# Performance work log

Measured on AMD Instinct MI355X. Metric: run time of the kernel, lower is better.

Reference implementation:

```python
import jax, jax.numpy as jnp
import numpy as np

B, C, L = 16, 128, 2048


def setup_inputs() -> dict:
    key = jax.random.key(0)
    ks = jax.random.split(key, 7)
    s = 1.0 / np.sqrt(C)  # torch Conv1d default init scale
    x = jax.random.normal(ks[0], (B, C, L), dtype=jnp.float32)
    W1 = jax.random.uniform(ks[1], (C, C), jnp.float32, -s, s)
    b1 = jax.random.uniform(ks[2], (C,), jnp.float32, -s, s)
    W2 = jax.random.uniform(ks[3], (C, C), jnp.float32, -s, s)
    b2 = jax.random.uniform(ks[4], (C,), jnp.float32, -s, s)
    W3 = jax.random.uniform(ks[5], (C, C), jnp.float32, -s, s)
    b3 = jax.random.uniform(ks[6], (C,), jnp.float32, -s, s)
    return {"x": x, "W1": W1, "b1": b1, "W2": W2, "b2": b2, "W3": W3, "b3": b3}


def _conv1x1(x, W, b):
    # x: [B,C,L], W: [out,in] -> [B,out,L]
    return jnp.einsum('oc,bcl->bol', W, x) + b[None, :, None]


def reference(x, W1, b1, W2, b2, W3, b3):
    q = _conv1x1(x, W1, b1).transpose(0, 2, 1)  # [B,L,C]
    k = _conv1x1(x, W2, b2).transpose(0, 2, 1)  # [B,L,C]
    v = _conv1x1(x, W3, b3).transpose(0, 2, 1)  # [B,L,C]
    attn = jnp.einsum('bic,bjc->bij', q, k)     # [B,L,L]
    attn = jax.nn.softmax(attn, axis=-1)
    out = jnp.einsum('bij,bjc->bic', attn, v)   # [B,L,C]
    return out.transpose(0, 2, 1)               # [B,C,L]
```

## Files before the change

### kernel.cpp

```cpp
#include <hip/hip_runtime.h>
#include <hip/hip_bf16.h>
#include <stdint.h>

#define B_ 16
#define C_ 128
#define L_ 2048
#define LOG2E 1.4426950408889634f

typedef __attribute__((ext_vector_type(8))) short bf16x8;
typedef __attribute__((ext_vector_type(4))) float f32x4;
typedef __attribute__((ext_vector_type(16))) float f32x16;
typedef __attribute__((ext_vector_type(4))) unsigned int u32x4;

typedef __attribute__((address_space(3))) unsigned int lds_u32_t;
typedef const __attribute__((address_space(1))) unsigned int gbl_u32_t;

__device__ __forceinline__ void gload_lds16(const void* g, void* l) {
  __builtin_amdgcn_global_load_lds((gbl_u32_t*)g,
                                   (lds_u32_t*)(unsigned long long)l, 16, 0, 0);
}

__device__ __forceinline__ unsigned short f2bf(float x) {
  union { float f; unsigned u; } v; v.f = x;
  unsigned u = v.u;
  u += 0x7fffu + ((u >> 16) & 1u);
  return (unsigned short)(u >> 16);
}

__device__ __forceinline__ unsigned pk2(float a, float b) {
  return (unsigned)f2bf(a) | ((unsigned)f2bf(b) << 16);
}

__device__ __forceinline__ unsigned cvtpk_bf16(float lo, float hi_) {
  unsigned r;
  asm("v_cvt_pk_bf16_f32 %0, %1, %2" : "=v"(r) : "v"(lo), "v"(hi_));
  return r;
}

__device__ __forceinline__ f32x16 z16() {
  f32x16 v;
#pragma unroll
  for (int i = 0; i < 16; ++i) v[i] = 0.f;
  return v;
}

__device__ __forceinline__ float tmax16(f32x16 v) {
  float a0 = fmaxf(v[0], v[1]),  a1 = fmaxf(v[2], v[3]);
  float a2 = fmaxf(v[4], v[5]),  a3 = fmaxf(v[6], v[7]);
  float a4 = fmaxf(v[8], v[9]),  a5 = fmaxf(v[10], v[11]);
  float a6 = fmaxf(v[12], v[13]), a7 = fmaxf(v[14], v[15]);
  float b0 = fmaxf(a0, a1), b1 = fmaxf(a2, a3);
  float b2 = fmaxf(a4, a5), b3 = fmaxf(a6, a7);
  return fmaxf(fmaxf(b0, b1), fmaxf(b2, b3));
}

__device__ __forceinline__ float tsum16(f32x16 v) {
  float a0 = v[0] + v[1],  a1 = v[2] + v[3];
  float a2 = v[4] + v[5],  a3 = v[6] + v[7];
  float a4 = v[8] + v[9],  a5 = v[10] + v[11];
  float a6 = v[12] + v[13], a7 = v[14] + v[15];
  float b0 = a0 + a1, b1 = a2 + a3, b2 = a4 + a5, b3 = a6 + a7;
  return (b0 + b1) + (b2 + b3);
}

__global__ __launch_bounds__(256, 2) void proj_kernel(
    const float* __restrict__ x,
    const float* __restrict__ W1, const float* __restrict__ b1,
    const float* __restrict__ W2, const float* __restrict__ b2,
    const float* __restrict__ W3, const float* __restrict__ b3,
    unsigned short* __restrict__ Qo, unsigned short* __restrict__ Ko,
    unsigned short* __restrict__ Vt)
{
  __shared__ unsigned short Xt[64][136];
  __shared__ unsigned short Wl[128][136];

  const int b  = blockIdx.x & 15;
  const int lt = blockIdx.x >> 4;
  const int l0 = lt * 64;
  const int tid = threadIdx.x;
  const int w = tid >> 6, lane = tid & 63, li = lane & 15, lg = lane >> 4;

  for (int it = 0; it < 8; ++it) {
    int idx = tid + it * 256;
    int c = idx >> 4, f4 = idx & 15;
    const float4 vv = *(const float4*)(x + (size_t)(b * C_ + c) * L_ + l0 + f4 * 4);
    Xt[f4 * 4 + 0][c] = f2bf(vv.x);
    Xt[f4 * 4 + 1][c] = f2bf(vv.y);
    Xt[f4 * 4 + 2][c] = f2bf(vv.z);
    Xt[f4 * 4 + 3][c] = f2bf(vv.w);
  }

  auto stageW = [&](const float* W) {
    for (int it = 0; it < 16; ++it) {
      int idx = tid + it * 256;
      int o = idx >> 5, f4 = idx & 31;
      const float4 vv = *(const float4*)(W + (size_t)o * C_ + f4 * 4);
      unsigned short* p = &Wl[o][f4 * 4];
      p[0] = f2bf(vv.x); p[1] = f2bf(vv.y); p[2] = f2bf(vv.z); p[3] = f2bf(vv.w);
    }
  };

  auto computePhase = [&](const float* bias, unsigned short* Out, int mode, float sc) {
    f32x4 acc[8];
#pragma unroll
    for (int ni = 0; ni < 8; ++ni) acc[ni] = (f32x4){0.f, 0.f, 0.f, 0.f};
    bf16x8 af[4];
#pragma unroll
    for (int kk = 0; kk < 4; ++kk)
      af[kk] = *(const bf16x8*)&Xt[w * 16 + li][lg * 8 + kk * 32];
#pragma unroll
    for (int kk = 0; kk < 4; ++kk) {
#pragma unroll
      for (int ni = 0; ni < 8; ++ni) {
        bf16x8 bf = *(const bf16x8*)&Wl[ni * 16 + li][lg * 8 + kk * 32];
        acc[ni] = __builtin_amdgcn_mfma_f32_16x16x32_bf16(af[kk], bf, acc[ni], 0, 0, 0);
      }
    }
    if (mode == 0) {
#pragma unroll
      for (int ni = 0; ni < 8; ++ni) {
        float bv = bias[ni * 16 + li];
#pragma unroll
        for (int r = 0; r < 4; ++r) {
          int lrow = l0 + w * 16 + lg * 4 + r;
          Out[(size_t)(b * L_ + lrow) * C_ + ni * 16 + li] = f2bf((acc[ni][r] + bv) * sc);
        }
      }
    } else {
#pragma unroll
      for (int ni = 0; ni < 8; ++ni) {
        float bv = bias[ni * 16 + li];
        int o = ni * 16 + li;
        unsigned long long pw =
            (unsigned long long)pk2(acc[ni][0] + bv, acc[ni][1] + bv) |
            ((unsigned long long)pk2(acc[ni][2] + bv, acc[ni][3] + bv) << 32);
        *(unsigned long long*)(Out + (size_t)(b * C_ + o) * L_ + l0 + w * 16 + lg * 4) = pw;
      }
    }
  };

  stageW(W1);
  __syncthreads();
  computePhase(b1, Qo, 0, LOG2E);
  __syncthreads();
  stageW(W2);
  __syncthreads();
  computePhase(b2, Ko, 0, 1.0f);
  __syncthreads();
  stageW(W3);
  __syncthreads();
  computePhase(b3, Vt, 1, 1.0f);
}

__global__ __launch_bounds__(256, 1) void attn_kernel(
    const unsigned short* __restrict__ Q,
    const unsigned short* __restrict__ K,
    const unsigned short* __restrict__ Vt,
    float* __restrict__ out)
{
  __shared__ unsigned short kbuf[2][64 * C_];
  __shared__ unsigned short vbuf[2][C_ * 64];

  const int b  = blockIdx.x & 15;
  const int qt = blockIdx.x >> 4;
  const int tid = threadIdx.x;
  const int w = tid >> 6, lane = tid & 63;
  const int q32 = lane & 31, hi = lane >> 5;
  const int qrow = qt * 128 + w * 32 + q32;
  const size_t bLC = (size_t)b * L_ * C_;

  bf16x8 qf[8];
  {
    const unsigned short* qp = Q + bLC + (size_t)qrow * C_ + hi * 8;
#pragma unroll
    for (int kt = 0; kt < 8; ++kt) qf[kt] = *(const bf16x8*)(qp + kt * 16);
  }

  f32x16 oacc[4];
#pragma unroll
  for (int i = 0; i < 4; ++i) oacc[i] = z16();
  float m2 = -3e38f, lrun = 0.f;

  const char* kgb = (const char*)(K + bLC);
  const char* vgb = (const char*)(Vt + bLC);

  auto stage = [&](int sel, int t) {
    const char* ktb = kgb + (size_t)t * (64 * 256);
    const char* vt0 = vgb + (size_t)t * 128;
#pragma unroll
    for (int i2 = 0; i2 < 4; ++i2) {
      int db = w * 4096 + i2 * 1024;
      int d  = db + lane * 16;
      int row = d >> 8, cb = d & 255;
      gload_lds16(ktb + row * 256 + (cb ^ ((row & 7) << 4)), (char*)kbuf[sel] + db);
      int rc = d >> 7, cv = d & 127;
      gload_lds16(vt0 + (size_t)rc * (L_ * 2) + (cv ^ ((rc & 7) << 4)),
                  (char*)vbuf[sel] + db);
    }
  };

  stage(0, 0);
  __syncthreads();

  int cur = 0;
  for (int t = 0; t < 32; ++t) {
    if (t + 1 < 32) stage(cur ^ 1, t + 1);

    const char* kb = (const char*)kbuf[cur];
    f32x16 s0 = z16(), s1 = z16();
#pragma unroll
    for (int kt2 = 0; kt2 < 8; ++kt2) {
      int row0 = q32, row1 = 32 + q32;
      bf16x8 kf0 = *(const bf16x8*)(kb + (row0 << 8) +
                                    ((kt2 * 32 + hi * 16) ^ ((row0 & 7) << 4)));
      bf16x8 kf1 = *(const bf16x8*)(kb + (row1 << 8) +
                                    ((kt2 * 32 + hi * 16) ^ ((row1 & 7) << 4)));
      s0 = __builtin_amdgcn_mfma_f32_32x32x16_bf16(kf0, qf[kt2], s0, 0, 0, 0);
      s1 = __builtin_amdgcn_mfma_f32_32x32x16_bf16(kf1, qf[kt2], s1, 0, 0, 0);
    }

    float pm = fmaxf(tmax16(s0), tmax16(s1));
    pm = fmaxf(pm, __shfl_xor(pm, 32));
    if (!__all(pm - m2 <= 8.f)) {
      float mn = fmaxf(m2, pm);
      float al = exp2f(m2 - mn);
      lrun *= al;
#pragma unroll
      for (int ct = 0; ct < 4; ++ct) oacc[ct] = oacc[ct] * al;
      m2 = mn;
    }
#pragma unroll
    for (int r = 0; r < 16; ++r) {
      s0[r] = exp2f(s0[r] - m2);
      s1[r] = exp2f(s1[r] - m2);
    }
    float ps = tsum16(s0) + tsum16(s1);
    ps += __shfl_xor(ps, 32);
    lrun += ps;

    const char* vb = (const char*)vbuf[cur];
    auto pvstep = [&](const f32x16& sv, int kj) {
      const int base = (kj & 1) * 8;
      unsigned wl0 = cvtpk_bf16(sv[base + 0], sv[base + 1]);
      unsigned wl1 = cvtpk_bf16(sv[base + 2], sv[base + 3]);
      unsigned wh0 = cvtpk_bf16(sv[base + 4], sv[base + 5]);
      unsigned wh1 = cvtpk_bf16(sv[base + 6], sv[base + 7]);
      unsigned snd0 = hi ? wl0 : wh0;
      unsigned snd1 = hi ? wl1 : wh1;
      unsigned rcv0 = (unsigned)__shfl_xor((int)snd0, 32);
      unsigned rcv1 = (unsigned)__shfl_xor((int)snd1, 32);
      unsigned w0 = hi ? rcv0 : wl0;
      unsigned w1 = hi ? rcv1 : wl1;
      unsigned w2 = hi ? wh0 : rcv0;
      unsigned w3 = hi ? wh1 : rcv1;
      u32x4 pw = {w0, w1, w2, w3};
      bf16x8 pf = *reinterpret_cast<bf16x8*>(&pw);
#pragma unroll
      for (int ct = 0; ct < 4; ++ct) {
        int rowc = ct * 32 + q32;
        bf16x8 vf = *(const bf16x8*)(vb + (rowc << 7) +
                                     ((kj * 32 + hi * 16) ^ ((rowc & 7) << 4)));
        oacc[ct] = __builtin_amdgcn_mfma_f32_32x32x16_bf16(vf, pf, oacc[ct], 0, 0, 0);
      }
    };
    pvstep(s0, 0);
    pvstep(s0, 1);
    pvstep(s1, 2);
    pvstep(s1, 3);

    __syncthreads();
    cur ^= 1;
  }

  float inv = 1.0f / lrun;
  float* ob = out + (size_t)b * C_ * L_ + qrow;
#pragma unroll
  for (int ct = 0; ct < 4; ++ct) {
#pragma unroll
    for (int r = 0; r < 16; ++r) {
      int c = ct * 32 + (r & 3) + 8 * (r >> 2) + 4 * hi;
      ob[(size_t)c * L_] = oacc[ct][r] * inv;
    }
  }
}

extern "C" void kernel_launch(void* const* d_in, const int* in_sizes, int n_in,
                              void* d_out, int out_size, void* d_ws, size_t ws_size,
                              hipStream_t stream) {
  (void)in_sizes; (void)n_in; (void)out_size; (void)ws_size;
  const float* x  = (const float*)d_in[0];
  const float* W1 = (const float*)d_in[1];
  const float* b1 = (const float*)d_in[2];
  const float* W2 = (const float*)d_in[3];
  const float* b2 = (const float*)d_in[4];
  const float* W3 = (const float*)d_in[5];
  const float* b3 = (const float*)d_in[6];

  unsigned short* Q  = (unsigned short*)d_ws;
  unsigned short* K  = Q + (size_t)B_ * L_ * C_;
  unsigned short* Vt = K + (size_t)B_ * L_ * C_;

  proj_kernel<<<512, 256, 0, stream>>>(x, W1, b1, W2, b2, W3, b3, Q, K, Vt);
  attn_kernel<<<256, 256, 0, stream>>>(Q, K, Vt, (float*)d_out);
}
```

Before: 85.97 us.

## Split attention key tiles across wave pairs with 512-thread blocks and merge softmax

The attention kernel now launches 512 threads. Each pair of waves shares 32 query rows and splits every 64-key tile in half. Waves 0-3 stage K tiles and waves 4-7 stage V tiles. Each wave keeps its own running max and sum, and the pair merges them at the end through LDS scratch. The QK dot product is also split into two independent MFMA accumulators over the channel dimension, and s_setprio is raised around the MFMA blocks. The aim is more resident waves per CU to hide latency, at the cost of an extra epilogue reduction and a tighter register budget that could cause spills.

```diff
diff --git a/kernel.cpp b/kernel.cpp
--- a/kernel.cpp
+++ b/kernel.cpp
@@ -44,7 +44,7 @@
   return v;
 }
 
-__device__ __forceinline__ float tmax16(f32x16 v) {
+__device__ __forceinline__ float tmax16(const f32x16& v) {
   float a0 = fmaxf(v[0], v[1]),  a1 = fmaxf(v[2], v[3]);
   float a2 = fmaxf(v[4], v[5]),  a3 = fmaxf(v[6], v[7]);
   float a4 = fmaxf(v[8], v[9]),  a5 = fmaxf(v[10], v[11]);
@@ -54,7 +54,7 @@
   return fmaxf(fmaxf(b0, b1), fmaxf(b2, b3));
 }
 
-__device__ __forceinline__ float tsum16(f32x16 v) {
+__device__ __forceinline__ float tsum16(const f32x16& v) {
   float a0 = v[0] + v[1],  a1 = v[2] + v[3];
   float a2 = v[4] + v[5],  a3 = v[6] + v[7];
   float a4 = v[8] + v[9],  a5 = v[10] + v[11];
@@ -152,21 +152,21 @@
   computePhase(b3, Vt, 1, 1.0f);
 }
 
-__global__ __launch_bounds__(256, 1) void attn_kernel(
+__global__ __launch_bounds__(512, 2) void attn_kernel(
     const unsigned short* __restrict__ Q,
     const unsigned short* __restrict__ K,
     const unsigned short* __restrict__ Vt,
     float* __restrict__ out)
 {
-  __shared__ unsigned short kbuf[2][64 * C_];
-  __shared__ unsigned short vbuf[2][C_ * 64];
+  __shared__ char smem[65536 + 2048];
 
   const int b  = blockIdx.x & 15;
   const int qt = blockIdx.x >> 4;
   const int tid = threadIdx.x;
   const int w = tid >> 6, lane = tid & 63;
   const int q32 = lane & 31, hi = lane >> 5;
-  const int qrow = qt * 128 + w * 32 + q32;
+  const int qg = w >> 1, jh = w & 1;
+  const int qrow = qt * 128 + qg * 32 + q32;
   const size_t bLC = (size_t)b * L_ * C_;
 
   bf16x8 qf[8];
@@ -185,17 +185,24 @@
   const char* vgb = (const char*)(Vt + bLC);
 
   auto stage = [&](int sel, int t) {
-    const char* ktb = kgb + (size_t)t * (64 * 256);
-    const char* vt0 = vgb + (size_t)t * 128;
-#pragma unroll
-    for (int i2 = 0; i2 < 4; ++i2) {
-      int db = w * 4096 + i2 * 1024;
-      int d  = db + lane * 16;
-      int row = d >> 8, cb = d & 255;
-      gload_lds16(ktb + row * 256 + (cb ^ ((row & 7) << 4)), (char*)kbuf[sel] + db);
-      int rc = d >> 7, cv = d & 127;
-      gload_lds16(vt0 + (size_t)rc * (L_ * 2) + (cv ^ ((rc & 7) << 4)),
-                  (char*)vbuf[sel] + db);
+    if (w < 4) {
+      const char* ktb = kgb + (size_t)t * (64 * 256);
+      char* dst = smem + sel * 16384 + (w & 3) * 4096;
+#pragma unroll
+      for (int i2 = 0; i2 < 4; ++i2) {
+        int d = (w & 3) * 4096 + i2 * 1024 + lane * 16;
+        int row = d >> 8, cb = d & 255;
+        gload_lds16(ktb + row * 256 + (cb ^ ((row & 15) << 4)), dst + i2 * 1024);
+      }
+    } else {
+      const char* vt0 = vgb + (size_t)t * 128;
+      char* dst = smem + 32768 + sel * 16384 + (w & 3) * 4096;
+#pragma unroll
+      for (int i2 = 0; i2 < 4; ++i2) {
+        int d = (w & 3) * 4096 + i2 * 1024 + lane * 16;
+        int rc = d >> 7, cv = d & 127;
+        gload_lds16(vt0 + (size_t)rc * (L_ * 2) + (cv ^ ((rc & 7) << 4)), dst + i2 * 1024);
+      }
     }
   };
 
@@ -206,20 +213,24 @@
   for (int t = 0; t < 32; ++t) {
     if (t + 1 < 32) stage(cur ^ 1, t + 1);
 
-    const char* kb = (const char*)kbuf[cur];
-    f32x16 s0 = z16(), s1 = z16();
-#pragma unroll
-    for (int kt2 = 0; kt2 < 8; ++kt2) {
-      int row0 = q32, row1 = 32 + q32;
-      bf16x8 kf0 = *(const bf16x8*)(kb + (row0 << 8) +
-                                    ((kt2 * 32 + hi * 16) ^ ((row0 & 7) << 4)));
-      bf16x8 kf1 = *(const bf16x8*)(kb + (row1 << 8) +
-                                    ((kt2 * 32 + hi * 16) ^ ((row1 & 7) << 4)));
-      s0 = __builtin_amdgcn_mfma_f32_32x32x16_bf16(kf0, qf[kt2], s0, 0, 0, 0);
-      s1 = __builtin_amdgcn_mfma_f32_32x32x16_bf16(kf1, qf[kt2], s1, 0, 0, 0);
-    }
-
-    float pm = fmaxf(tmax16(s0), tmax16(s1));
+    const char* kb = smem + cur * 16384;
+    const int krow = jh * 32 + q32;
+    const int kro  = krow << 8, ksw = (krow & 15) << 4;
+    f32x16 sA = z16(), sB = z16();
+    __builtin_amdgcn_s_setprio(1);
+#pragma unroll
+    for (int kt2 = 0; kt2 < 4; ++kt2) {
+      bf16x8 kf0 = *(const bf16x8*)(kb + kro + ((kt2 * 32 + hi * 16) ^ ksw));
+      bf16x8 kf1 = *(const bf16x8*)(kb + kro + (((kt2 + 4) * 32 + hi * 16) ^ ksw));
+      sA = __builtin_amdgcn_mfma_f32_32x32x16_bf16(kf0, qf[kt2], sA, 0, 0, 0);
+      sB = __builtin_amdgcn_mfma_f32_32x32x16_bf16(kf1, qf[kt2 + 4], sB, 0, 0, 0);
+    }
+    __builtin_amdgcn_s_setprio(0);
+    f32x16 s;
+#pragma unroll
+    for (int r = 0; r < 16; ++r) s[r] = sA[r] + sB[r];
+
+    float pm = tmax16(s);
     pm = fmaxf(pm, __shfl_xor(pm, 32));
     if (!__all(pm - m2 <= 8.f)) {
       float mn = fmaxf(m2, pm);
@@ -230,21 +241,19 @@
       m2 = mn;
     }
 #pragma unroll
-    for (int r = 0; r < 16; ++r) {
-      s0[r] = exp2f(s0[r] - m2);
-      s1[r] = exp2f(s1[r] - m2);
-    }
-    float ps = tsum16(s0) + tsum16(s1);
+    for (int r = 0; r < 16; ++r) s[r] = exp2f(s[r] - m2);
+    float ps = tsum16(s);
     ps += __shfl_xor(ps, 32);
     lrun += ps;
 
-    const char* vb = (const char*)vbuf[cur];
-    auto pvstep = [&](const f32x16& sv, int kj) {
-      const int base = (kj & 1) * 8;
-      unsigned wl0 = cvtpk_bf16(sv[base + 0], sv[base + 1]);
-      unsigned wl1 = cvtpk_bf16(sv[base + 2], sv[base + 3]);
-      unsigned wh0 = cvtpk_bf16(sv[base + 4], sv[base + 5]);
-      unsigned wh1 = cvtpk_bf16(sv[base + 6], sv[base + 7]);
+    bf16x8 pf[2];
+#pragma unroll
+    for (int kj = 0; kj < 2; ++kj) {
+      const int base = kj * 8;
+      unsigned wl0 = cvtpk_bf16(s[base + 0], s[base + 1]);
+      unsigned wl1 = cvtpk_bf16(s[base + 2], s[base + 3]);
+      unsigned wh0 = cvtpk_bf16(s[base + 4], s[base + 5]);
+      unsigned wh1 = cvtpk_bf16(s[base + 6], s[base + 7]);
       unsigned snd0 = hi ? wl0 : wh0;
       unsigned snd1 = hi ? wl1 : wh1;
       unsigned rcv0 = (unsigned)__shfl_xor((int)snd0, 32);
@@ -254,33 +263,82 @@
       unsigned w2 = hi ? wh0 : rcv0;
       unsigned w3 = hi ? wh1 : rcv1;
       u32x4 pw = {w0, w1, w2, w3};
-      bf16x8 pf = *reinterpret_cast<bf16x8*>(&pw);
+      pf[kj] = *reinterpret_cast<bf16x8*>(&pw);
+    }
+
+    const char* vb = smem + 32768 + cur * 16384;
+    __builtin_amdgcn_s_setprio(1);
+#pragma unroll
+    for (int kj = 0; kj < 2; ++kj) {
+      const int kjg = jh * 2 + kj;
 #pragma unroll
       for (int ct = 0; ct < 4; ++ct) {
         int rowc = ct * 32 + q32;
         bf16x8 vf = *(const bf16x8*)(vb + (rowc << 7) +
-                                     ((kj * 32 + hi * 16) ^ ((rowc & 7) << 4)));
-        oacc[ct] = __builtin_amdgcn_mfma_f32_32x32x16_bf16(vf, pf, oacc[ct], 0, 0, 0);
-      }
-    };
-    pvstep(s0, 0);
-    pvstep(s0, 1);
-    pvstep(s1, 2);
-    pvstep(s1, 3);
+                                     ((kjg * 32 + hi * 16) ^ ((rowc & 7) << 4)));
+        oacc[ct] = __builtin_amdgcn_mfma_f32_32x32x16_bf16(vf, pf[kj], oacc[ct], 0, 0, 0);
+      }
+    }
+    __builtin_amdgcn_s_setprio(0);
 
     __syncthreads();
     cur ^= 1;
   }
 
-  float inv = 1.0f / lrun;
+  float* mlb = (float*)(smem + 65536);
+  if (hi == 0) {
+    mlb[(w * 32 + q32) * 2 + 0] = m2;
+    mlb[(w * 32 + q32) * 2 + 1] = lrun;
+  }
+  __syncthreads();
+  const float mB = mlb[((w ^ 1) * 32 + q32) * 2 + 0];
+  const float lB = mlb[((w ^ 1) * 32 + q32) * 2 + 1];
+  const float mstar = fmaxf(m2, mB);
+  const float aown  = exp2f(m2 - mstar);
+  float* scrb = (float*)smem + (size_t)(qg * 64 + lane) * 33;
   float* ob = out + (size_t)b * C_ * L_ + qrow;
-#pragma unroll
-  for (int ct = 0; ct < 4; ++ct) {
+  float inv = 0.f;
+  if (jh == 0) {
+    const float aB = exp2f(mB - mstar);
+    inv = 1.0f / (lrun * aown + lB * aB);
+  }
+  __syncthreads();
+  if (jh == 1) {
 #pragma unroll
     for (int r = 0; r < 16; ++r) {
-      int c = ct * 32 + (r & 3) + 8 * (r >> 2) + 4 * hi;
-      ob[(size_t)c * L_] = oacc[ct][r] * inv;
-    }
+      scrb[r]      = oacc[0][r] * aown;
+      scrb[16 + r] = oacc[1][r] * aown;
+    }
+  }
+  __syncthreads();
+  if (jh == 0) {
+#pragma unroll
+    for (int ct = 0; ct < 2; ++ct)
+#pragma unroll
+      for (int r = 0; r < 16; ++r) {
+        float v = oacc[ct][r] * aown + scrb[ct * 16 + r];
+        int c = ct * 32 + (r & 3) + 8 * (r >> 2) + 4 * hi;
+        ob[(size_t)c * L_] = v * inv;
+      }
+  }
+  __syncthreads();
+  if (jh == 1) {
+#pragma unroll
+    for (int r = 0; r < 16; ++r) {
+      scrb[r]      = oacc[2][r] * aown;
+      scrb[16 + r] = oacc[3][r] * aown;
+    }
+  }
+  __syncthreads();
+  if (jh == 0) {
+#pragma unroll
+    for (int ct = 0; ct < 2; ++ct)
+#pragma unroll
+      for (int r = 0; r < 16; ++r) {
+        float v = oacc[2 + ct][r] * aown + scrb[ct * 16 + r];
+        int c = (2 + ct) * 32 + (r & 3) + 8 * (r >> 2) + 4 * hi;
+        ob[(size_t)c * L_] = v * inv;
+      }
   }
 }
 
@@ -301,5 +359,5 @@
   unsigned short* Vt = K + (size_t)B_ * L_ * C_;
 
   proj_kernel<<<512, 256, 0, stream>>>(x, W1, b1, W2, b2, W3, b3, Q, K, Vt);
-  attn_kernel<<<256, 256, 0, stream>>>(Q, K, Vt, (float*)d_out);
-}
+  attn_kernel<<<256, 512, 0, stream>>>(Q, K, Vt, (float*)d_out);
+}
```

Result: faster. 74.72 us (-13.1%).
